# Kernel tuning notes

Measured on AMD Instinct MI355X. Metric: run time of the kernel, lower is better.

Reference implementation:

```python
import jax, jax.numpy as jnp
import numpy as np

N, E = 50000, 800000
D_IN, D_H, D_OUT = 128, 128, 128


def setup_inputs() -> dict:
    key = jax.random.key(0)
    ks = jax.random.split(key, 8)
    x = jax.random.normal(ks[0], (N, D_IN), dtype=jnp.float32)
    edge_index = jax.random.randint(ks[1], (2, E), 0, N, dtype=jnp.int64)
    s_in = 1.0 / np.sqrt(D_IN)
    s_h = 1.0 / np.sqrt(D_H)
    W1 = jax.random.normal(ks[2], (D_IN, D_H), dtype=jnp.float32) * s_in
    b1 = jnp.zeros((D_H,), jnp.float32)
    Wg = jax.random.normal(ks[3], (D_H, D_H), dtype=jnp.float32) * s_h
    bg = jnp.zeros((D_H,), jnp.float32)
    W2 = jax.random.normal(ks[4], (D_H, D_OUT), dtype=jnp.float32) * s_h
    b2 = jnp.zeros((D_OUT,), jnp.float32)
    return {"x": x, "edge_index": edge_index, "W1": W1, "b1": b1,
            "Wg": Wg, "bg": bg, "W2": W2, "b2": b2}


def reference(x, edge_index, W1, b1, Wg, bg, W2, b2):
    # Linear -> ReLU
    h = jax.nn.relu(x @ W1 + b1)                      # [N, D_H]
    # GCNConv: transform, add self-loops, sym-normalize, scatter-aggregate
    h = h @ Wg                                        # [N, D_H]
    row, col = edge_index[0], edge_index[1]
    loop = jnp.arange(N, dtype=edge_index.dtype)
    row = jnp.concatenate([row, loop])                # [E+N] sources
    col = jnp.concatenate([col, loop])                # [E+N] targets
    deg = jax.ops.segment_sum(jnp.ones(E + N, h.dtype), col, num_segments=N)
    dinv = jnp.where(deg > 0, jax.lax.rsqrt(deg), 0.0)
    norm = dinv[row] * dinv[col]                      # [E+N]
    agg = jax.ops.segment_sum(h[row] * norm[:, None], col, num_segments=N)
    agg = agg + bg                                    # GCNConv bias
    # ReLU -> Linear
    return jax.nn.relu(agg) @ W2 + b2                 # [N, D_OUT]
```

## Files before the change

### kernel.cpp

```cpp
#include <hip/hip_runtime.h>

#define D 128

typedef short bf16x8 __attribute__((ext_vector_type(8)));
typedef float f32x4 __attribute__((ext_vector_type(4)));

static __device__ __forceinline__ unsigned int f2bf(float f) {
  unsigned int u = __float_as_uint(f);
  return (u + 0x7FFFu + ((u >> 16) & 1u)) >> 16;
}
static __device__ __forceinline__ unsigned int pack2bf(float lo, float hi) {
  return f2bf(lo) | (f2bf(hi) << 16);
}
static __device__ __forceinline__ float bf_lo(unsigned int v) {
  return __uint_as_float(v << 16);
}
static __device__ __forceinline__ float bf_hi(unsigned int v) {
  return __uint_as_float(v & 0xFFFF0000u);
}


__global__ __launch_bounds__(256) void k_zero(int* __restrict__ p, int n) {
  int i = blockIdx.x * 256 + threadIdx.x;
  if (i < n) p[i] = 0;
}

__global__ __launch_bounds__(256) void k_fill(const int* __restrict__ ei, int E,
                                              int* __restrict__ deg,
                                              unsigned short* __restrict__ csr16,
                                              int cap) {
  int e = blockIdx.x * 256 + threadIdx.x;
  if (e < E) {
    int r = __builtin_nontemporal_load(ei + e);
    int c = __builtin_nontemporal_load(ei + E + e);
    int pos = atomicAdd(&deg[c], 1);
    if (pos < cap)
      csr16[(size_t)c * cap + pos] = (unsigned short)r;
  }
}

__global__ __launch_bounds__(256) void k_dinv(const int* __restrict__ deg, int N,
                                              float* __restrict__ dinv) {
  int n = blockIdx.x * 256 + threadIdx.x;
  if (n < N) dinv[n] = rsqrtf((float)(deg[n] + 1));
}


__global__ __launch_bounds__(256) void k_wcvt(const float* __restrict__ W1,
                                              const float* __restrict__ Wg,
                                              const float* __restrict__ W2,
                                              unsigned short* __restrict__ WT) {
  const float* W = (blockIdx.x == 0) ? W1 : (blockIdx.x == 1) ? Wg : W2;
  unsigned short* T = WT + blockIdx.x * 16384;
  for (int idx = threadIdx.x; idx < 16384; idx += 256) {
    int k = idx >> 7, j = idx & 127;
    T[j * 128 + k] = (unsigned short)f2bf(W[idx]);
  }
}


__global__ __launch_bounds__(256) void k_mlp(const float* __restrict__ x,
                                             const unsigned short* __restrict__ W1T,
                                             const float* __restrict__ b1,
                                             const unsigned short* __restrict__ WgT,
                                             const float* __restrict__ dinv,
                                             unsigned short* __restrict__ h2, int N) {
  __shared__ unsigned short xs[64][136];
  __shared__ unsigned short wB[128][136];
  const int t = threadIdx.x;
  const int wave = t >> 6, lane = t & 63;
  const int rowBase = blockIdx.x * 64;
  const int ar = lane & 15, kg = lane >> 4;

#pragma unroll
  for (int i = 0; i < 8; ++i) {
    int idx = t + i * 256;
    int r = idx >> 5, c4 = (idx & 31) << 2;
    float4 v = make_float4(0.f, 0.f, 0.f, 0.f);
    int gr = rowBase + r;
    if (gr < N) v = *(const float4*)(x + (size_t)gr * D + c4);
    *(unsigned int*)&xs[r][c4]     = pack2bf(v.x, v.y);
    *(unsigned int*)&xs[r][c4 + 2] = pack2bf(v.z, v.w);
  }
#pragma unroll
  for (int i = 0; i < 8; ++i) {
    int idx = t + i * 256;
    int r = idx >> 4, c8 = (idx & 15) << 3;
    *(uint4*)&wB[r][c8] = *(const uint4*)(W1T + r * 128 + c8);
  }
  __syncthreads();

  float bias1[8];
#pragma unroll
  for (int cf = 0; cf < 8; ++cf) bias1[cf] = b1[cf * 16 + ar];
  float dnv[4];
#pragma unroll
  for (int reg = 0; reg < 4; ++reg) {
    int gr = rowBase + wave * 16 + 4 * kg + reg;
    dnv[reg] = (gr < N) ? dinv[gr] : 0.f;
  }

  f32x4 acc[8];
#pragma unroll
  for (int cf = 0; cf < 8; ++cf) acc[cf] = (f32x4){0.f, 0.f, 0.f, 0.f};
#pragma unroll
  for (int ks = 0; ks < 4; ++ks) {
    bf16x8 a = *(const bf16x8*)&xs[wave * 16 + ar][ks * 32 + kg * 8];
#pragma unroll
    for (int cf = 0; cf < 8; ++cf) {
      bf16x8 b = *(const bf16x8*)&wB[cf * 16 + ar][ks * 32 + kg * 8];
      acc[cf] = __builtin_amdgcn_mfma_f32_16x16x32_bf16(a, b, acc[cf], 0, 0, 0);
    }
  }

#pragma unroll
  for (int cf = 0; cf < 8; ++cf)
#pragma unroll
    for (int reg = 0; reg < 4; ++reg) {
      float v = fmaxf(acc[cf][reg] + bias1[cf], 0.f);
      xs[wave * 16 + 4 * kg + reg][cf * 16 + ar] = (unsigned short)f2bf(v);
    }
  __syncthreads();

#pragma unroll
  for (int i = 0; i < 8; ++i) {
    int idx = t + i * 256;
    int r = idx >> 4, c8 = (idx & 15) << 3;
    *(uint4*)&wB[r][c8] = *(const uint4*)(WgT + r * 128 + c8);
  }
  __syncthreads();

#pragma unroll
  for (int cf = 0; cf < 8; ++cf) acc[cf] = (f32x4){0.f, 0.f, 0.f, 0.f};
#pragma unroll
  for (int ks = 0; ks < 4; ++ks) {
    bf16x8 a = *(const bf16x8*)&xs[wave * 16 + ar][ks * 32 + kg * 8];
#pragma unroll
    for (int cf = 0; cf < 8; ++cf) {
      bf16x8 b = *(const bf16x8*)&wB[cf * 16 + ar][ks * 32 + kg * 8];
      acc[cf] = __builtin_amdgcn_mfma_f32_16x16x32_bf16(a, b, acc[cf], 0, 0, 0);
    }
  }

#pragma unroll
  for (int cf = 0; cf < 8; ++cf)
#pragma unroll
    for (int reg = 0; reg < 4; ++reg) {
      int gr = rowBase + wave * 16 + 4 * kg + reg;
      if (gr < N)
        h2[(size_t)gr * D + cf * 16 + ar] = (unsigned short)f2bf(acc[cf][reg] * dnv[reg]);
    }
}


__global__ __launch_bounds__(256) void k_agg(const unsigned short* __restrict__ h2,
                                             const int* __restrict__ deg,
                                             const unsigned short* __restrict__ csr16,
                                             const float* __restrict__ dinv,
                                             const float* __restrict__ bg,
                                             float* __restrict__ agg, int N, int cap) {
  int wave = threadIdx.x >> 6;
  int lane = threadIdx.x & 63;
  int n = blockIdx.x * 4 + wave;
  if (n >= N) return;
  const unsigned int* h2v = (const unsigned int*)h2;
  float dn = dinv[n];
  float ax = 0.f, ay = 0.f;
  int cnt = min(deg[n], cap);
  size_t base = (size_t)n * cap;
  int i = 0;
  for (; i + 8 <= cnt; i += 8) {
    uint4 pk = *(const uint4*)(csr16 + base + i);
    int s[8] = {(int)(pk.x & 0xFFFFu), (int)(pk.x >> 16),
                (int)(pk.y & 0xFFFFu), (int)(pk.y >> 16),
                (int)(pk.z & 0xFFFFu), (int)(pk.z >> 16),
                (int)(pk.w & 0xFFFFu), (int)(pk.w >> 16)};
    unsigned int v[8];
#pragma unroll
    for (int u = 0; u < 8; ++u) v[u] = h2v[(size_t)s[u] * 64 + lane];
#pragma unroll
    for (int u = 0; u < 8; ++u) { ax += bf_lo(v[u]); ay += bf_hi(v[u]); }
  }
  for (; i < cnt; ++i) {
    int s = csr16[base + i];
    unsigned int v = h2v[(size_t)s * 64 + lane];
    ax += bf_lo(v); ay += bf_hi(v);
  }
  {
    unsigned int v = h2v[(size_t)n * 64 + lane];
    ax += bf_lo(v); ay += bf_hi(v);
  }
  float2 bgv = ((const float2*)bg)[lane];
  float2 o;
  o.x = fmaxf(fmaf(ax, dn, bgv.x), 0.f);
  o.y = fmaxf(fmaf(ay, dn, bgv.y), 0.f);
  ((float2*)agg)[(size_t)n * 64 + lane] = o;
}


__global__ __launch_bounds__(256) void k_out(const float* __restrict__ a,
                                             const unsigned short* __restrict__ W2T,
                                             const float* __restrict__ b2,
                                             float* __restrict__ out, int N) {
  __shared__ unsigned short xs[64][136];
  __shared__ unsigned short wB[128][136];
  const int t = threadIdx.x;
  const int wave = t >> 6, lane = t & 63;
  const int rowBase = blockIdx.x * 64;
  const int ar = lane & 15, kg = lane >> 4;

#pragma unroll
  for (int i = 0; i < 8; ++i) {
    int idx = t + i * 256;
    int r = idx >> 5, c4 = (idx & 31) << 2;
    float4 v = make_float4(0.f, 0.f, 0.f, 0.f);
    int gr = rowBase + r;
    if (gr < N) v = *(const float4*)(a + (size_t)gr * D + c4);
    *(unsigned int*)&xs[r][c4]     = pack2bf(v.x, v.y);
    *(unsigned int*)&xs[r][c4 + 2] = pack2bf(v.z, v.w);
  }
#pragma unroll
  for (int i = 0; i < 8; ++i) {
    int idx = t + i * 256;
    int r = idx >> 4, c8 = (idx & 15) << 3;
    *(uint4*)&wB[r][c8] = *(const uint4*)(W2T + r * 128 + c8);
  }
  __syncthreads();

  float bias2[8];
#pragma unroll
  for (int cf = 0; cf < 8; ++cf) bias2[cf] = b2[cf * 16 + ar];

  f32x4 acc[8];
#pragma unroll
  for (int cf = 0; cf < 8; ++cf) acc[cf] = (f32x4){0.f, 0.f, 0.f, 0.f};
#pragma unroll
  for (int ks = 0; ks < 4; ++ks) {
    bf16x8 a8 = *(const bf16x8*)&xs[wave * 16 + ar][ks * 32 + kg * 8];
#pragma unroll
    for (int cf = 0; cf < 8; ++cf) {
      bf16x8 b8 = *(const bf16x8*)&wB[cf * 16 + ar][ks * 32 + kg * 8];
      acc[cf] = __builtin_amdgcn_mfma_f32_16x16x32_bf16(a8, b8, acc[cf], 0, 0, 0);
    }
  }

#pragma unroll
  for (int cf = 0; cf < 8; ++cf)
#pragma unroll
    for (int reg = 0; reg < 4; ++reg) {
      int gr = rowBase + wave * 16 + 4 * kg + reg;
      if (gr < N)
        out[(size_t)gr * D + cf * 16 + ar] = acc[cf][reg] + bias2[cf];
    }
}


extern "C" void kernel_launch(void* const* d_in, const int* in_sizes, int n_in,
                              void* d_out, int out_size, void* d_ws, size_t ws_size,
                              hipStream_t stream) {
  const float* x  = (const float*)d_in[0];
  const int*   ei = (const int*)d_in[1];
  const float* W1 = (const float*)d_in[2];
  const float* b1 = (const float*)d_in[3];
  const float* Wg = (const float*)d_in[4];
  const float* bg = (const float*)d_in[5];
  const float* W2 = (const float*)d_in[6];
  const float* b2 = (const float*)d_in[7];
  const int N = in_sizes[0] / D;
  const int E = in_sizes[1] / 2;
  float* out = (float*)d_out;

  unsigned short* h2 = (unsigned short*)d_ws;
  unsigned short* WT = h2 + (size_t)N * D;
  float* dinv = (float*)(WT + 3 * 16384);
  int*   deg  = (int*)(dinv + N);
  unsigned short* csr16 = (unsigned short*)(deg + N);

  size_t fixed = (size_t)N * D * 2 + 3 * 16384 * 2 + (size_t)N * 8;
  int cap;
  if (ws_size >= fixed + (size_t)N * 64 * 2)      cap = 64;
  else if (ws_size >= fixed + (size_t)N * 48 * 2) cap = 48;
  else return;

  k_zero<<<(N + 255) / 256, 256, 0, stream>>>(deg, N);
  k_fill<<<(E + 255) / 256, 256, 0, stream>>>(ei, E, deg, csr16, cap);
  k_dinv<<<(N + 255) / 256, 256, 0, stream>>>(deg, N, dinv);
  k_wcvt<<<3, 256, 0, stream>>>(W1, Wg, W2, WT);
  k_mlp <<<(N + 63) / 64, 256, 0, stream>>>(x, WT, b1, WT + 16384, dinv, h2, N);
  k_agg <<<(N + 3) / 4, 256, 0, stream>>>(h2, deg, csr16, dinv, bg, out, N, cap);
  k_out <<<(N + 63) / 64, 256, 0, stream>>>(out, WT + 2 * 16384, b2, out, N);
}
```

Before: 149.8 us.

## Bucket edges by destination partition before building CSR to localize atomics

Adds a pre-pass that bins edges into 8 destination-range partitions through a shared-memory local sort with per-block global offsets, packing source and destination into one 32-bit word. A second kernel then builds the per-node CSR from each partition, with the block index interleaved across partitions. The aim is to concentrate the scattered atomicAdds on deg and the csr16 writes into smaller address ranges for better cache locality. The cost is an extra kernel launch plus an extra write and read of the edge list, and the 16-bit packing assumes node ids fit in 16 bits, which N=50000 does.

```diff
diff --git a/kernel.cpp b/kernel.cpp
--- a/kernel.cpp
+++ b/kernel.cpp
@@ -1,6 +1,7 @@
 #include <hip/hip_runtime.h>
 
 #define D 128
+#define NPART 8
 
 typedef short bf16x8 __attribute__((ext_vector_type(8)));
 typedef float f32x4 __attribute__((ext_vector_type(4)));
@@ -23,6 +24,61 @@
 __global__ __launch_bounds__(256) void k_zero(int* __restrict__ p, int n) {
   int i = blockIdx.x * 256 + threadIdx.x;
   if (i < n) p[i] = 0;
+}
+
+__global__ __launch_bounds__(256) void k_part(const int* __restrict__ ei, int E, int N,
+                                              unsigned int* __restrict__ parts, int cap_p,
+                                              int* __restrict__ pcur) {
+  __shared__ unsigned int buf[256];
+  __shared__ int cnt[NPART], base[NPART + 1], gbase[NPART];
+  const int t = threadIdx.x;
+  const int e = blockIdx.x * 256 + t;
+  if (t < NPART) cnt[t] = 0;
+  __syncthreads();
+  const int npb = (N + NPART - 1) / NPART;
+  int bin = -1, lpos = 0;
+  unsigned int pk = 0;
+  if (e < E) {
+    int s = __builtin_nontemporal_load(ei + e);
+    int d = __builtin_nontemporal_load(ei + E + e);
+    bin = d / npb;
+    pk = ((unsigned int)d << 16) | (unsigned int)s;
+    lpos = atomicAdd(&cnt[bin], 1);
+  }
+  __syncthreads();
+  if (t == 0) {
+    int run = 0;
+    for (int b = 0; b < NPART; ++b) { base[b] = run; run += cnt[b]; }
+    base[NPART] = run;
+  }
+  __syncthreads();
+  if (t < NPART && cnt[t] > 0) gbase[t] = atomicAdd(&pcur[t], cnt[t]);
+  __syncthreads();
+  if (bin >= 0) buf[base[bin] + lpos] = pk;
+  __syncthreads();
+  const int total = base[NPART];
+  if (t < total) {
+    int b = 0;
+    while (t >= base[b + 1]) ++b;
+    int off = gbase[b] + (t - base[b]);
+    if (off < cap_p) parts[(size_t)b * cap_p + off] = buf[t];
+  }
+}
+
+__global__ __launch_bounds__(256) void k_fill2(const unsigned int* __restrict__ parts, int cap_p,
+                                               const int* __restrict__ pcur,
+                                               int* __restrict__ deg,
+                                               unsigned short* __restrict__ csr16, int cap) {
+  const int p = blockIdx.x & (NPART - 1);
+  const int i = (blockIdx.x / NPART) * 256 + threadIdx.x;
+  const int cnt = pcur[p];
+  if (i < cnt && i < cap_p) {
+    unsigned int pk = parts[(size_t)p * cap_p + i];
+    int d = (int)(pk >> 16), s = (int)(pk & 0xFFFFu);
+    int pos = atomicAdd(&deg[d], 1);
+    if (pos < cap)
+      csr16[(size_t)d * cap + pos] = (unsigned short)s;
+  }
 }
 
 __global__ __launch_bounds__(256) void k_fill(const int* __restrict__ ei, int E,
@@ -274,16 +330,29 @@
   unsigned short* WT = h2 + (size_t)N * D;
   float* dinv = (float*)(WT + 3 * 16384);
   int*   deg  = (int*)(dinv + N);
-  unsigned short* csr16 = (unsigned short*)(deg + N);
-
-  size_t fixed = (size_t)N * D * 2 + 3 * 16384 * 2 + (size_t)N * 8;
-  int cap;
-  if (ws_size >= fixed + (size_t)N * 64 * 2)      cap = 64;
-  else if (ws_size >= fixed + (size_t)N * 48 * 2) cap = 48;
+  int*   pcur = deg + N;
+  unsigned short* csr16 = (unsigned short*)(pcur + NPART);
+
+  const int cap_p = E / NPART + 8192;
+  size_t fixed = (size_t)N * D * 2 + 3 * 16384 * 2 + (size_t)N * 8 + NPART * 4;
+  size_t parts_b = (size_t)NPART * cap_p * 4;
+
+  int cap, use_part;
+  if (ws_size >= fixed + (size_t)N * 64 * 2 + parts_b)      { cap = 64; use_part = 1; }
+  else if (ws_size >= fixed + (size_t)N * 64 * 2)           { cap = 64; use_part = 0; }
+  else if (ws_size >= fixed + (size_t)N * 48 * 2)           { cap = 48; use_part = 0; }
   else return;
 
-  k_zero<<<(N + 255) / 256, 256, 0, stream>>>(deg, N);
-  k_fill<<<(E + 255) / 256, 256, 0, stream>>>(ei, E, deg, csr16, cap);
+  unsigned int* parts = (unsigned int*)(csr16 + (size_t)N * cap);
+
+  k_zero<<<(N + NPART + 255) / 256, 256, 0, stream>>>(deg, N + NPART);
+  if (use_part) {
+    k_part <<<(E + 255) / 256, 256, 0, stream>>>(ei, E, N, parts, cap_p, pcur);
+    int bpp = (cap_p + 255) / 256;
+    k_fill2<<<NPART * bpp, 256, 0, stream>>>(parts, cap_p, pcur, deg, csr16, cap);
+  } else {
+    k_fill <<<(E + 255) / 256, 256, 0, stream>>>(ei, E, deg, csr16, cap);
+  }
   k_dinv<<<(N + 255) / 256, 256, 0, stream>>>(deg, N, dinv);
   k_wcvt<<<3, 256, 0, stream>>>(W1, Wg, W2, WT);
   k_mlp <<<(N + 63) / 64, 256, 0, stream>>>(x, WT, b1, WT + 16384, dinv, h2, N);
```

After: 173.6 us. 1.16x slower.
